# Kernel optimization log

Measured on AMD Instinct MI355X. Metric: run time of the kernel, lower is better.

## Reference

```python
import jax, jax.numpy as jnp
import numpy as np

N_FEATURE = 1024
N_HEAD = 16
DK = N_FEATURE // N_HEAD
SCALE = float(np.sqrt(DK))
LN_EPS = 1e-5


def setup_inputs() -> dict:
    key = jax.random.key(0)
    ks = jax.random.split(key, 12)
    B, T, F = 4, 2048, N_FEATURE
    s = 1.0 / np.sqrt(F)
    inp = {
        "key": jax.random.normal(ks[0], (B, T, F), jnp.float32),
        "value": jax.random.normal(ks[1], (B, T, F), jnp.float32),
        "query": jax.random.normal(ks[2], (B, T, F), jnp.float32),
        "Wq": jax.random.uniform(ks[3], (F, F), jnp.float32, -s, s),
        "bq": jax.random.uniform(ks[4], (F,), jnp.float32, -s, s),
        "Wk": jax.random.uniform(ks[5], (F, F), jnp.float32, -s, s),
        "bk": jax.random.uniform(ks[6], (F,), jnp.float32, -s, s),
        "Wv": jax.random.uniform(ks[7], (F, F), jnp.float32, -s, s),
        "bv": jax.random.uniform(ks[8], (F,), jnp.float32, -s, s),
        "Wo": jax.random.uniform(ks[9], (F, F), jnp.float32, -s, s),
        "bo": jax.random.uniform(ks[10], (F,), jnp.float32, -s, s),
        "ln_g": jnp.ones((F,), jnp.float32),
        "ln_b": jnp.zeros((F,), jnp.float32),
    }
    return inp


def reference(key, value, query, Wq, bq, Wk, bk, Wv, bv, Wo, bo, ln_g, ln_b):
    # key/value/query: [B, T, F]. torch chunk(n_head, -1) == reshape to (B,T,H,dk).
    B, T, F = query.shape
    residual = query
    q = (query @ Wq.T + bq).reshape(B, T, N_HEAD, DK)
    k = (key @ Wk.T + bk).reshape(B, T, N_HEAD, DK)
    v = (value @ Wv.T + bv).reshape(B, T, N_HEAD, DK)
    # scores: [B, H, Tq, Tk]
    scores = jnp.einsum("bqhd,bkhd->bhqk", q, k) / SCALE
    attn = jax.nn.softmax(scores, axis=-1)
    ctx = jnp.einsum("bhqk,bkhd->bqhd", attn, v).reshape(B, T, F)
    out = ctx @ Wo.T + bo  # dropout in eval mode = identity
    x = residual + out
    mu = jnp.mean(x, axis=-1, keepdims=True)
    var = jnp.mean(jnp.square(x - mu), axis=-1, keepdims=True)
    return (x - mu) * jax.lax.rsqrt(var + LN_EPS) * ln_g + ln_b
```

## Files before the change

kernel.cpp:

```cpp
#include <hip/hip_runtime.h>
#include <hip/hip_bf16.h>
#include <cstdint>
#include <cstddef>

#define DEVI __device__ __forceinline__

typedef __attribute__((ext_vector_type(8))) short short8;
typedef __attribute__((ext_vector_type(4))) float f32x4;
typedef __attribute__((ext_vector_type(16))) float f32x16;
typedef __attribute__((ext_vector_type(4))) unsigned int u32x4;

constexpr int Bz = 4, Tt = 2048, Fd = 1024, Hh = 16, Dk = 64;
constexpr int Mrows = Bz * Tt;
constexpr float QSCALE = 0.18033688011112042f;

DEVI unsigned short f2bf(float f) {
  union { __hip_bfloat16 h; unsigned short u; } cv;
  cv.h = __float2bfloat16(f);
  return cv.u;
}

DEVI unsigned cvtpk(float a, float b) {
  unsigned r;
  asm("v_cvt_pk_bf16_f32 %0, %1, %2" : "=v"(r) : "v"(a), "v"(b));
  return r;
}

DEVI void gl_lds16(const void* g, void* s) {
  __builtin_amdgcn_global_load_lds(
      (const __attribute__((address_space(1))) void*)g,
      (__attribute__((address_space(3))) void*)s, 16, 0, 0);
}

__global__ void cvt4_bf16(const float* __restrict__ s0, unsigned short* __restrict__ d0,
                          const float* __restrict__ s1, unsigned short* __restrict__ d1,
                          const float* __restrict__ s2, unsigned short* __restrict__ d2,
                          const float* __restrict__ s3, unsigned short* __restrict__ d3,
                          int n4) {
  const float* src = blockIdx.y == 0 ? s0 : (blockIdx.y == 1 ? s1 : (blockIdx.y == 2 ? s2 : s3));
  unsigned short* dst = blockIdx.y == 0 ? d0 : (blockIdx.y == 1 ? d1 : (blockIdx.y == 2 ? d2 : d3));
  int i = blockIdx.x * blockDim.x + threadIdx.x;
  int stride = gridDim.x * blockDim.x;
  for (; i < n4; i += stride) {
    float4 v = reinterpret_cast<const float4*>(src)[i];
    ushort4 o;
    o.x = f2bf(v.x); o.y = f2bf(v.y); o.z = f2bf(v.z); o.w = f2bf(v.w);
    reinterpret_cast<ushort4*>(dst)[i] = o;
  }
}

__global__ __launch_bounds__(256, 2) void gemm_qkvf(
    const float* __restrict__ q32, const float* __restrict__ k32,
    const float* __restrict__ v32, const unsigned short* __restrict__ wq,
    const unsigned short* __restrict__ wk, const unsigned short* __restrict__ wv,
    const float* __restrict__ bq, const float* __restrict__ bk, const float* __restrict__ bv,
    unsigned short* __restrict__ Qb, unsigned short* __restrict__ Kb,
    unsigned short* __restrict__ Vt) {
  constexpr int K = 1024, N = 1024;
  __shared__ __align__(16) unsigned short As[128 * 64];
  __shared__ __align__(16) unsigned short Bs[128 * 64];
  int z = blockIdx.z;
  const float* A32 = z == 0 ? q32 : (z == 1 ? k32 : v32);
  const unsigned short* W = z == 0 ? wq : (z == 1 ? wk : wv);
  const float* bias = z == 0 ? bq : (z == 1 ? bk : bv);
  void* out = z == 0 ? (void*)Qb : (z == 1 ? (void*)Kb : (void*)Vt);
  float scale = z == 0 ? QSCALE : 1.0f;
  int mode = z == 2 ? 2 : 0;

  int f = blockIdx.y * gridDim.x + blockIdx.x;
  f = (f & 7) * 64 + (f >> 3);
  const int m0 = (f >> 3) * 128, n0 = (f & 7) * 128;
  const int t = threadIdx.x, w = t >> 6, l = t & 63;
  const int wr = w >> 1, wc = w & 1;
  const int lr = l & 15, lg = l >> 4;
  f32x4 acc[4][4] = {};

  for (int k0 = 0; k0 < K; k0 += 64) {
    __syncthreads();
    float4 fA[4][2];
#pragma unroll
    for (int i = 0; i < 4; ++i) {
      int row = i * 32 + w * 8 + (l >> 3);
      const float* src = A32 + (size_t)(m0 + row) * K + k0 + (l & 7) * 8;
      fA[i][0] = ((const float4*)src)[0];
      fA[i][1] = ((const float4*)src)[1];
    }
#pragma unroll
    for (int i = 0; i < 4; ++i) {
      int base = i * 4096 + w * 1024;
      int d = base + l * 16;
      int row = d >> 7;
      int srcb = ((l & 7) ^ (row & 7)) << 4;
      gl_lds16((const char*)W + ((size_t)(n0 + row) * K + k0) * 2 + srcb, (char*)Bs + base);
    }
#pragma unroll
    for (int i = 0; i < 4; ++i) {
      int row = i * 32 + w * 8 + (l >> 3);
      u32x4 wv4;
      wv4[0] = cvtpk(fA[i][0].x, fA[i][0].y);
      wv4[1] = cvtpk(fA[i][0].z, fA[i][0].w);
      wv4[2] = cvtpk(fA[i][1].x, fA[i][1].y);
      wv4[3] = cvtpk(fA[i][1].z, fA[i][1].w);
      int slot = (l & 7) ^ (row & 7);
      *(u32x4*)((char*)As + row * 128 + slot * 16) = wv4;
    }
    __syncthreads();
#pragma unroll
    for (int kk = 0; kk < 2; ++kk) {
      short8 af[4], bf[4];
#pragma unroll
      for (int i = 0; i < 4; ++i) {
        int ra = wr * 64 + i * 16 + lr;
        int rb = wc * 64 + i * 16 + lr;
        af[i] = *(const short8*)((const char*)As + ra * 128 + (((kk * 4 + lg) ^ (ra & 7)) << 4));
        bf[i] = *(const short8*)((const char*)Bs + rb * 128 + (((kk * 4 + lg) ^ (rb & 7)) << 4));
      }
#pragma unroll
      for (int mi = 0; mi < 4; ++mi)
#pragma unroll
        for (int ni = 0; ni < 4; ++ni)
          acc[mi][ni] = __builtin_amdgcn_mfma_f32_16x16x32_bf16(af[mi], bf[ni], acc[mi][ni], 0, 0, 0);
    }
  }
#pragma unroll
  for (int mi = 0; mi < 4; ++mi)
#pragma unroll
    for (int ni = 0; ni < 4; ++ni) {
      int col = n0 + wc * 64 + ni * 16 + lr;
      float bv = bias[col];
      if (mode == 2) {
        int hh = col >> 6, dd = col & 63;
        int row = m0 + wr * 64 + mi * 16 + lg * 4;
        int bb = row >> 11, t0 = row & 2047;
        ushort4 o;
        o.x = f2bf(acc[mi][ni][0] + bv);
        o.y = f2bf(acc[mi][ni][1] + bv);
        o.z = f2bf(acc[mi][ni][2] + bv);
        o.w = f2bf(acc[mi][ni][3] + bv);
        *(ushort4*)((unsigned short*)out + (((size_t)(bb * Hh + hh) * Dk + dd) << 11) + t0) = o;
      } else {
#pragma unroll
        for (int r = 0; r < 4; ++r) {
          int row = m0 + wr * 64 + mi * 16 + lg * 4 + r;
          ((unsigned short*)out)[(size_t)row * N + col] = f2bf((acc[mi][ni][r] + bv) * scale);
        }
      }
    }
}

__global__ __launch_bounds__(256, 2) void gemm_out(
    const unsigned short* __restrict__ A, const unsigned short* __restrict__ W,
    const float* __restrict__ bias, const float* __restrict__ resid,
    float* __restrict__ out) {
  constexpr int K = 1024, N = 1024;
  __shared__ __align__(16) unsigned short As[128 * 64];
  __shared__ __align__(16) unsigned short Bs[128 * 64];
  int f = blockIdx.y * gridDim.x + blockIdx.x;
  f = (f & 7) * 64 + (f >> 3);
  const int m0 = (f >> 3) * 128, n0 = (f & 7) * 128;
  const int t = threadIdx.x, w = t >> 6, l = t & 63;
  const int wr = w >> 1, wc = w & 1;
  const int lr = l & 15, lg = l >> 4;
  f32x4 acc[4][4] = {};
  for (int k0 = 0; k0 < K; k0 += 64) {
    __syncthreads();
#pragma unroll
    for (int i = 0; i < 4; ++i) {
      int base = i * 4096 + w * 1024;
      int d = base + l * 16;
      int row = d >> 7;
      int srcb = ((l & 7) ^ (row & 7)) << 4;
      gl_lds16((const char*)A + ((size_t)(m0 + row) * K + k0) * 2 + srcb, (char*)As + base);
      gl_lds16((const char*)W + ((size_t)(n0 + row) * K + k0) * 2 + srcb, (char*)Bs + base);
    }
    __syncthreads();
#pragma unroll
    for (int kk = 0; kk < 2; ++kk) {
      short8 af[4], bf[4];
#pragma unroll
      for (int i = 0; i < 4; ++i) {
        int ra = wr * 64 + i * 16 + lr;
        int rb = wc * 64 + i * 16 + lr;
        af[i] = *(const short8*)((const char*)As + ra * 128 + (((kk * 4 + lg) ^ (ra & 7)) << 4));
        bf[i] = *(const short8*)((const char*)Bs + rb * 128 + (((kk * 4 + lg) ^ (rb & 7)) << 4));
      }
#pragma unroll
      for (int mi = 0; mi < 4; ++mi)
#pragma unroll
        for (int ni = 0; ni < 4; ++ni)
          acc[mi][ni] = __builtin_amdgcn_mfma_f32_16x16x32_bf16(af[mi], bf[ni], acc[mi][ni], 0, 0, 0);
    }
  }
#pragma unroll
  for (int mi = 0; mi < 4; ++mi)
#pragma unroll
    for (int ni = 0; ni < 4; ++ni) {
      int col = n0 + wc * 64 + ni * 16 + lr;
      float bv = bias[col];
#pragma unroll
      for (int r = 0; r < 4; ++r) {
        int row = m0 + wr * 64 + mi * 16 + lg * 4 + r;
        size_t idx = (size_t)row * N + col;
        out[idx] = acc[mi][ni][r] + bv + resid[idx];
      }
    }
}

__global__ __launch_bounds__(512, 2) void attn_kernel(
    const unsigned short* __restrict__ Qb, const unsigned short* __restrict__ Kb,
    const unsigned short* __restrict__ Vt, unsigned short* __restrict__ Ctx) {
  __shared__ __align__(16) unsigned short smem[8 * 4096];
  int bid = blockIdx.x;
  const int xcd = bid & 7, idx = bid >> 3;
  const int bh = xcd * 8 + (idx >> 2);
  const int q0 = (idx & 3) * 512;
  const int h = bh & 15;
  const int b = bh >> 4;
  const int t = threadIdx.x, w = t >> 6, l = t & 63;
  const int q31 = l & 31, hi = l >> 5;
  const int qbase = q0 + w * 64;

  short8 qfA[4], qfB[4];
  {
    const unsigned short* qpA = Qb + (size_t)(b * Tt + qbase + q31) * Fd + h * Dk;
    const unsigned short* qpB = qpA + (size_t)32 * Fd;
#pragma unroll
    for (int c = 0; c < 4; ++c) {
      qfA[c] = *(const short8*)(qpA + c * 16 + hi * 8);
      qfB[c] = *(const short8*)(qpB + c * 16 + hi * 8);
    }
  }

  int koff[8];
#pragma unroll
  for (int g = 0; g < 2; ++g)
#pragma unroll
    for (int c = 0; c < 4; ++c) {
      int row = g * 32 + q31;
      koff[g * 4 + c] = row * 128 + ((c * 32 + hi * 16) ^ ((row & 7) << 4));
    }

  const size_t kbase = (size_t)(b * Tt) * Fd + h * Dk;
  const size_t vbase = (size_t)((b * Hh + h) * Dk) * Tt;

  f32x16 OA0{}, OA1{}, OB0{}, OB1{};
  short8 pfA[4], pfB[4];
  float lsA0 = 0.f, lsB0 = 0.f, lsA1 = 0.f, lsB1 = 0.f;

  auto kbuf = [&](int kt) { return (const char*)smem + ((kt & 3) << 13); };
  auto vbuf = [&](int kt) { return (const char*)smem + 32768 + ((kt & 3) << 13); };

  auto stage = [&](int kt) {
    char* Kd = (char*)smem + ((kt & 3) << 13);
    char* Vd = (char*)smem + 32768 + ((kt & 3) << 13);
    int base = w * 1024;
    int d0 = base + l * 16;
    int row = d0 >> 7, inb = d0 & 127;
    int srcb = inb ^ ((row & 7) << 4);
    gl_lds16((const char*)Kb + (kbase + (size_t)(kt * 64 + row) * Fd) * 2 + srcb, Kd + base);
    gl_lds16((const char*)Vt + (vbase + (size_t)row * Tt + kt * 64) * 2 + srcb, Vd + base);
  };

  auto qk = [&](int kt, f32x16& S0a, f32x16& S1a, f32x16& S0b, f32x16& S1b) {
    const char* Kd = kbuf(kt);
    __builtin_amdgcn_s_setprio(1);
#pragma unroll
    for (int c = 0; c < 4; ++c) {
      short8 k0 = *(const short8*)(Kd + koff[c]);
      short8 k1 = *(const short8*)(Kd + koff[4 + c]);
      S0a = __builtin_amdgcn_mfma_f32_32x32x16_bf16(k0, qfA[c], S0a, 0, 0, 0);
      S1a = __builtin_amdgcn_mfma_f32_32x32x16_bf16(k1, qfA[c], S1a, 0, 0, 0);
      S0b = __builtin_amdgcn_mfma_f32_32x32x16_bf16(k0, qfB[c], S0b, 0, 0, 0);
      S1b = __builtin_amdgcn_mfma_f32_32x32x16_bf16(k1, qfB[c], S1b, 0, 0, 0);
    }
    __builtin_amdgcn_s_setprio(0);
  };

  auto pv = [&](int kt) {
    const char* Vd = vbuf(kt);
    __builtin_amdgcn_s_setprio(1);
#pragma unroll
    for (int db = 0; db < 2; ++db)
#pragma unroll
      for (int kvc = 0; kvc < 4; ++kvc) {
        short8 vf = *(const short8*)(Vd + koff[db * 4 + kvc]);
        if (db == 0) {
          OA0 = __builtin_amdgcn_mfma_f32_32x32x16_bf16(vf, pfA[kvc], OA0, 0, 0, 0);
          OB0 = __builtin_amdgcn_mfma_f32_32x32x16_bf16(vf, pfB[kvc], OB0, 0, 0, 0);
        } else {
          OA1 = __builtin_amdgcn_mfma_f32_32x32x16_bf16(vf, pfA[kvc], OA1, 0, 0, 0);
          OB1 = __builtin_amdgcn_mfma_f32_32x32x16_bf16(vf, pfB[kvc], OB1, 0, 0, 0);
        }
      }
    __builtin_amdgcn_s_setprio(0);
  };

  auto softmax_pack = [&](const f32x16& S0, const f32x16& S1, float& lsA, float& lsB, short8* pf) {
    unsigned pk0[8], pk1[8];
#pragma unroll
    for (int j = 0; j < 8; ++j) {
      int r = j * 2;
      float a0 = __builtin_amdgcn_exp2f(S0[r]);
      float a1 = __builtin_amdgcn_exp2f(S0[r + 1]);
      float b0 = __builtin_amdgcn_exp2f(S1[r]);
      float b1 = __builtin_amdgcn_exp2f(S1[r + 1]);
      lsA += a0 + a1;
      lsB += b0 + b1;
      pk0[j] = cvtpk(a0, a1);
      pk1[j] = cvtpk(b0, b1);
    }
#pragma unroll
    for (int kc = 0; kc < 2; ++kc) {
      unsigned a0 = pk0[kc * 4 + 0], a2 = pk0[kc * 4 + 2];
      unsigned a1 = pk0[kc * 4 + 1], a3 = pk0[kc * 4 + 3];
      asm("v_permlane32_swap_b32 %0, %1" : "+v"(a0), "+v"(a2));
      asm("v_permlane32_swap_b32 %0, %1" : "+v"(a1), "+v"(a3));
      unsigned b0 = pk1[kc * 4 + 0], b2 = pk1[kc * 4 + 2];
      unsigned b1 = pk1[kc * 4 + 1], b3 = pk1[kc * 4 + 3];
      asm("v_permlane32_swap_b32 %0, %1" : "+v"(b0), "+v"(b2));
      asm("v_permlane32_swap_b32 %0, %1" : "+v"(b1), "+v"(b3));
      u32x4 fa, fb;
      fa[0] = a0; fa[1] = a1; fa[2] = a2; fa[3] = a3;
      fb[0] = b0; fb[1] = b1; fb[2] = b2; fb[3] = b3;
      pf[kc] = __builtin_bit_cast(short8, fa);
      pf[2 + kc] = __builtin_bit_cast(short8, fb);
    }
  };

  stage(0);
  stage(1);
  asm volatile("s_waitcnt vmcnt(2)" ::: "memory");
  __builtin_amdgcn_s_barrier();
  stage(2);
  {
    f32x16 S0a{}, S1a{}, S0b{}, S1b{};
    qk(0, S0a, S1a, S0b, S1b);
    softmax_pack(S0a, S1a, lsA0, lsB0, pfA);
    softmax_pack(S0b, S1b, lsA1, lsB1, pfB);
  }
  for (int kt = 1; kt < 31; ++kt) {
    asm volatile("s_waitcnt vmcnt(2)" ::: "memory");
    __builtin_amdgcn_s_barrier();
    if (kt < 30) stage(kt + 2);
    f32x16 S0a{}, S1a{}, S0b{}, S1b{};
    qk(kt, S0a, S1a, S0b, S1b);
    pv(kt - 1);
    softmax_pack(S0a, S1a, lsA0, lsB0, pfA);
    softmax_pack(S0b, S1b, lsA1, lsB1, pfB);
  }
  asm volatile("s_waitcnt vmcnt(0)" ::: "memory");
  __builtin_amdgcn_s_barrier();
  {
    f32x16 S0a{}, S1a{}, S0b{}, S1b{};
    qk(31, S0a, S1a, S0b, S1b);
    pv(30);
    softmax_pack(S0a, S1a, lsA0, lsB0, pfA);
    softmax_pack(S0b, S1b, lsA1, lsB1, pfB);
  }
  pv(31);
  __builtin_amdgcn_s_barrier();

  float ls0 = lsA0 + lsB0;
  ls0 += __shfl_xor(ls0, 32);
  float linv0 = 1.0f / ls0;
  float ls1 = lsA1 + lsB1;
  ls1 += __shfl_xor(ls1, 32);
  float linv1 = 1.0f / ls1;
  unsigned short* Ow = smem + w * 4096;
#pragma unroll
  for (int g = 0; g < 2; ++g) {
    float linv = g == 0 ? linv0 : linv1;
    int rowq = g * 32 + q31;
#pragma unroll
    for (int db = 0; db < 2; ++db)
#pragma unroll
      for (int rp = 0; rp < 8; ++rp) {
        int r = rp * 2;
        float a, b2;
        if (g == 0) {
          a = (db == 0 ? OA0[r] : OA1[r]) * linv;
          b2 = (db == 0 ? OA0[r + 1] : OA1[r + 1]) * linv;
        } else {
          a = (db == 0 ? OB0[r] : OB1[r]) * linv;
          b2 = (db == 0 ? OB0[r + 1] : OB1[r + 1]) * linv;
        }
        unsigned wv = cvtpk(a, b2);
        int dd = db * 32 + (r & 3) + 8 * (r >> 2) + 4 * hi;
        int byteo = (rowq * 128 + (dd >> 1) * 4) ^ ((rowq & 7) << 4);
        *(unsigned*)((char*)Ow + byteo) = wv;
      }
  }
#pragma unroll
  for (int i = 0; i < 8; ++i) {
    int qq = i * 8 + (l >> 3), slot = l & 7;
    int byteo = (qq * 128 + slot * 16) ^ ((qq & 7) << 4);
    short8 ov = *(const short8*)((const char*)Ow + byteo);
    *(short8*)(Ctx + (size_t)(b * Tt + qbase + qq) * Fd + h * Dk + slot * 8) = ov;
  }
}

__global__ __launch_bounds__(256) void ln_res(
    float* __restrict__ xo, const float* __restrict__ gamma, const float* __restrict__ beta) {
  int row = blockIdx.x, t = threadIdx.x;
  float4 xv = ((const float4*)(xo + (size_t)row * Fd))[t];
  float x0 = xv.x, x1 = xv.y, x2 = xv.z, x3 = xv.w;
  float s = x0 + x1 + x2 + x3;
  float ss = x0 * x0 + x1 * x1 + x2 * x2 + x3 * x3;
#pragma unroll
  for (int off = 32; off >= 1; off >>= 1) {
    s += __shfl_xor(s, off);
    ss += __shfl_xor(ss, off);
  }
  __shared__ float rs_[4], rss[4];
  int w = t >> 6, l = t & 63;
  if (l == 0) { rs_[w] = s; rss[w] = ss; }
  __syncthreads();
  s = rs_[0] + rs_[1] + rs_[2] + rs_[3];
  ss = rss[0] + rss[1] + rss[2] + rss[3];
  float mu = s * (1.0f / 1024.0f);
  float var = ss * (1.0f / 1024.0f) - mu * mu;
  float rstd = rsqrtf(var + 1e-5f);
  float4 gv = ((const float4*)gamma)[t];
  float4 bv = ((const float4*)beta)[t];
  float4 o;
  o.x = (x0 - mu) * rstd * gv.x + bv.x;
  o.y = (x1 - mu) * rstd * gv.y + bv.y;
  o.z = (x2 - mu) * rstd * gv.z + bv.z;
  o.w = (x3 - mu) * rstd * gv.w + bv.w;
  ((float4*)(xo + (size_t)row * Fd))[t] = o;
}

extern "C" void kernel_launch(void* const* d_in, const int* in_sizes, int n_in,
                              void* d_out, int out_size, void* d_ws, size_t ws_size,
                              hipStream_t stream) {
  (void)in_sizes; (void)n_in; (void)out_size; (void)ws_size;
  const float* key   = (const float*)d_in[0];
  const float* value = (const float*)d_in[1];
  const float* query = (const float*)d_in[2];
  const float* Wq = (const float*)d_in[3];
  const float* bq = (const float*)d_in[4];
  const float* Wk = (const float*)d_in[5];
  const float* bk = (const float*)d_in[6];
  const float* Wv = (const float*)d_in[7];
  const float* bv_ = (const float*)d_in[8];
  const float* Wo = (const float*)d_in[9];
  const float* bo = (const float*)d_in[10];
  const float* ln_g = (const float*)d_in[11];
  const float* ln_b = (const float*)d_in[12];
  float* out = (float*)d_out;

  char* ws = (char*)d_ws;
  size_t off = 0;
  auto alloc = [&](size_t bytes) {
    char* p = ws + off;
    off += (bytes + 255) & ~(size_t)255;
    return p;
  };
  const size_t MF = (size_t)Mrows * Fd;
  unsigned short* Qb  = (unsigned short*)alloc(MF * 2);
  unsigned short* Kbf = (unsigned short*)alloc(MF * 2);
  unsigned short* Vtb = (unsigned short*)alloc(MF * 2);
  unsigned short* Ctx = (unsigned short*)alloc(MF * 2);
  unsigned short* wqb = (unsigned short*)alloc((size_t)Fd * Fd * 2);
  unsigned short* wkb = (unsigned short*)alloc((size_t)Fd * Fd * 2);
  unsigned short* wvb = (unsigned short*)alloc((size_t)Fd * Fd * 2);
  unsigned short* wob = (unsigned short*)alloc((size_t)Fd * Fd * 2);

  cvt4_bf16<<<dim3(256, 4), 256, 0, stream>>>(Wq, wqb, Wk, wkb, Wv, wvb, Wo, wob, (Fd * Fd) / 4);

  gemm_qkvf<<<dim3(Fd / 128, Mrows / 128, 3), 256, 0, stream>>>(
      query, key, value, wqb, wkb, wvb, bq, bk, bv_, Qb, Kbf, Vtb);

  attn_kernel<<<Bz * Hh * (Tt / 512), 512, 0, stream>>>(Qb, Kbf, Vtb, Ctx);

  gemm_out<<<dim3(Fd / 128, Mrows / 128), 256, 0, stream>>>(Ctx, wob, bo, query, out);
  ln_res<<<Mrows, 256, 0, stream>>>(out, ln_g, ln_b);
}
```

Baseline: 181.3 us.

## Deepen attention K/V LDS ring to eight stages and process two tiles per barrier

The K/V shared-memory ring in the attention kernel grows from 4 to 8 tile slots, and the prefetch distance grows to four tiles. The main loop now handles two key tiles per barrier/waitcnt step instead of one, which halves the number of block-wide barriers. The aim is more memory-latency hiding and less synchronisation. The cost is that LDS per block doubles to 128 KB, which likely no longer fits two blocks per CU and so lowers occupancy despite the launch bound.

```diff
diff --git a/kernel.cpp b/kernel.cpp
--- a/kernel.cpp
+++ b/kernel.cpp
@@ -209,7 +209,7 @@
 __global__ __launch_bounds__(512, 2) void attn_kernel(
     const unsigned short* __restrict__ Qb, const unsigned short* __restrict__ Kb,
     const unsigned short* __restrict__ Vt, unsigned short* __restrict__ Ctx) {
-  __shared__ __align__(16) unsigned short smem[8 * 4096];
+  __shared__ __align__(16) unsigned short smem[16 * 4096];
   int bid = blockIdx.x;
   const int xcd = bid & 7, idx = bid >> 3;
   const int bh = xcd * 8 + (idx >> 2);
@@ -247,12 +247,12 @@
   short8 pfA[4], pfB[4];
   float lsA0 = 0.f, lsB0 = 0.f, lsA1 = 0.f, lsB1 = 0.f;
 
-  auto kbuf = [&](int kt) { return (const char*)smem + ((kt & 3) << 13); };
-  auto vbuf = [&](int kt) { return (const char*)smem + 32768 + ((kt & 3) << 13); };
+  auto kbuf = [&](int kt) { return (const char*)smem + ((kt & 7) << 13); };
+  auto vbuf = [&](int kt) { return (const char*)smem + 65536 + ((kt & 7) << 13); };
 
   auto stage = [&](int kt) {
-    char* Kd = (char*)smem + ((kt & 3) << 13);
-    char* Vd = (char*)smem + 32768 + ((kt & 3) << 13);
+    char* Kd = (char*)smem + ((kt & 7) << 13);
+    char* Vd = (char*)smem + 65536 + ((kt & 7) << 13);
     int base = w * 1024;
     int d0 = base + l * 16;
     int row = d0 >> 7, inb = d0 & 127;
@@ -327,29 +327,51 @@
     }
   };
 
-  stage(0);
-  stage(1);
-  asm volatile("s_waitcnt vmcnt(2)" ::: "memory");
+  stage(0); stage(1); stage(2); stage(3);
+  asm volatile("s_waitcnt vmcnt(4)" ::: "memory");
   __builtin_amdgcn_s_barrier();
-  stage(2);
+  stage(4); stage(5);
   {
     f32x16 S0a{}, S1a{}, S0b{}, S1b{};
     qk(0, S0a, S1a, S0b, S1b);
     softmax_pack(S0a, S1a, lsA0, lsB0, pfA);
     softmax_pack(S0b, S1b, lsA1, lsB1, pfB);
   }
-  for (int kt = 1; kt < 31; ++kt) {
-    asm volatile("s_waitcnt vmcnt(2)" ::: "memory");
-    __builtin_amdgcn_s_barrier();
-    if (kt < 30) stage(kt + 2);
+  {
     f32x16 S0a{}, S1a{}, S0b{}, S1b{};
-    qk(kt, S0a, S1a, S0b, S1b);
-    pv(kt - 1);
+    qk(1, S0a, S1a, S0b, S1b);
+    pv(0);
     softmax_pack(S0a, S1a, lsA0, lsB0, pfA);
     softmax_pack(S0b, S1b, lsA1, lsB1, pfB);
   }
+  for (int p = 1; p < 15; ++p) {
+    asm volatile("s_waitcnt vmcnt(4)" ::: "memory");
+    __builtin_amdgcn_s_barrier();
+    if (p < 14) { stage(2 * p + 4); stage(2 * p + 5); }
+    {
+      f32x16 S0a{}, S1a{}, S0b{}, S1b{};
+      qk(2 * p, S0a, S1a, S0b, S1b);
+      pv(2 * p - 1);
+      softmax_pack(S0a, S1a, lsA0, lsB0, pfA);
+      softmax_pack(S0b, S1b, lsA1, lsB1, pfB);
+    }
+    {
+      f32x16 S0a{}, S1a{}, S0b{}, S1b{};
+      qk(2 * p + 1, S0a, S1a, S0b, S1b);
+      pv(2 * p);
+      softmax_pack(S0a, S1a, lsA0, lsB0, pfA);
+      softmax_pack(S0b, S1b, lsA1, lsB1, pfB);
+    }
+  }
   asm volatile("s_waitcnt vmcnt(0)" ::: "memory");
   __builtin_amdgcn_s_barrier();
+  {
+    f32x16 S0a{}, S1a{}, S0b{}, S1b{};
+    qk(30, S0a, S1a, S0b, S1b);
+    pv(29);
+    softmax_pack(S0a, S1a, lsA0, lsB0, pfA);
+    softmax_pack(S0b, S1b, lsA1, lsB1, pfB);
+  }
   {
     f32x16 S0a{}, S1a{}, S0b{}, S1b{};
     qk(31, S0a, S1a, S0b, S1b);
```

Result: no change. 180.9 us (-0.2%).
